# Optimization experiments

Hardware: AMD Instinct MI355X
Metric: run time of the kernel (lower is better)

The kernel has to match this reference:

```python
import jax, jax.numpy as jnp
import numpy as np

B, S, H, A = 64, 2048, 512, 512

def setup_inputs() -> dict:
    key = jax.random.key(0)
    k = jax.random.split(key, 8)
    s = 1.0 / np.sqrt(H)
    sa = 1.0 / np.sqrt(A)
    return {
        "decoder_output": jax.random.normal(k[0], (B, H), jnp.float32),
        "encoder_output": jax.random.normal(k[1], (B, S, H), jnp.float32),
        "W_dec": jax.random.uniform(k[2], (A, H), jnp.float32, -s, s),
        "b_dec": jax.random.uniform(k[3], (A,), jnp.float32, -s, s),
        "W_enc": jax.random.uniform(k[4], (A, H), jnp.float32, -s, s),
        "b_enc": jax.random.uniform(k[5], (A,), jnp.float32, -s, s),
        "V": jax.random.uniform(k[6], (1, A), jnp.float32, -sa, sa),
        "b_v": jax.random.uniform(k[7], (1,), jnp.float32, -sa, sa),
    }

def reference(decoder_output, encoder_output, W_dec, b_dec, W_enc, b_enc, V, b_v):
    # dec proj: (B, A); enc proj: (B, S, A)
    dec_p = decoder_output @ W_dec.T + b_dec
    enc_p = jnp.einsum('bsh,ah->bsa', encoder_output, W_enc) + b_enc
    h = jnp.tanh(dec_p[:, None, :] + enc_p)          # (B, S, A)
    scores = jnp.einsum('bsa,a->bs', h, V[0]) + b_v[0]  # (B, S)
    attn = jax.nn.softmax(scores, axis=-1)           # softmax over seq dim
    ctx = jnp.einsum('bs,bsh->bh', attn, encoder_output)  # (B, H)
    out = jnp.concatenate([ctx, decoder_output], axis=-1)  # (B, 2H)
    return out
```

## Files before the change

### kernel.cpp

```cpp
#include <hip/hip_runtime.h>
#include <cstdint>
#include <cstddef>

#define NB 64
#define NS 2048
#define NH 512
#define NA 512

#define BM 64
#define BK 32

typedef __attribute__((ext_vector_type(8))) short short8;
typedef __attribute__((ext_vector_type(4))) float f32x4;

__device__ inline short f2bf(float f) {
    union { float f; uint32_t u; } v; v.f = f;
    uint32_t u = v.u;
    uint32_t r = (u + 0x7fffu + ((u >> 16) & 1u)) >> 16;
    return (short)r;
}

__device__ inline uint32_t cvtpk_bf16(float lo, float hi) {
    uint32_t r;
    asm("v_cvt_pk_bf16_f32 %0, %1, %2" : "=v"(r) : "v"(lo), "v"(hi));
    return r;
}

__global__ __launch_bounds__(256) void k_decp(const float* __restrict__ dec,
                                              const float* __restrict__ Wd,
                                              const float* __restrict__ bd,
                                              const float* __restrict__ be,
                                              float* __restrict__ dp) {
    int b = blockIdx.x;
    __shared__ float dl[NH];
    for (int i = threadIdx.x; i < NH; i += 256) dl[i] = dec[b * NH + i];
    __syncthreads();
    for (int a = threadIdx.x; a < NA; a += 256) {
        const float4* wr = (const float4*)(Wd + (size_t)a * NH);
        float acc = 0.f;
#pragma unroll 8
        for (int h4 = 0; h4 < NH / 4; ++h4) {
            float4 w = wr[h4];
            acc += dl[h4*4+0]*w.x + dl[h4*4+1]*w.y + dl[h4*4+2]*w.z + dl[h4*4+3]*w.w;
        }
        dp[b * NA + a] = acc + bd[a] + be[a];
    }
}

__global__ __launch_bounds__(256) void k_packw(const float* __restrict__ We,
                                               short* __restrict__ wsw) {
    int t = blockIdx.x * 256 + threadIdx.x;
    int slot = t & 3;
    int a = (t >> 2) & (NA - 1);
    int kt = t >> 11;
    const float* src = We + (size_t)a * NH + kt * 32 + slot * 8;
    int dslot = slot ^ ((a >> 1) & 3);
    short* dst = wsw + (((size_t)kt * NA + a) * 4 + dslot) * 8;
    short8 o;
#pragma unroll
    for (int j = 0; j < 8; ++j) o[j] = f2bf(src[j]);
    *(short8*)dst = o;
}

__global__ __launch_bounds__(256, 2) void k_fused(const float* __restrict__ enc,
                                                  const short* __restrict__ wsw,
                                                  const float* __restrict__ dp,
                                                  const float* __restrict__ V,
                                                  float* __restrict__ pbuf,
                                                  float* __restrict__ ctxp) {
    __shared__ __align__(16) char smem[73728];

    const int tid = threadIdx.x;
    const int w = tid >> 6;
    const int l = tid & 63;
    const int lrow = l & 15;
    const int lg = l >> 4;
    const int row0 = blockIdx.x * BM;
    const int b = row0 >> 11;

    const int sa = tid >> 2;
    const int qa = tid & 3;
    const float* encs = enc + (size_t)(row0 + sa) * NH + qa * 8;
    const int aw_byte = (qa * 64 + (sa ^ (qa << 2))) * 16;

    const char* wsrc = (const char*)wsw;

    const int wfrag = ((w * 128 + lrow) * 4 + (lg ^ ((lrow >> 1) & 3))) * 16;
    const int afrag = (lg * 64 + (lrow ^ (lg << 2))) * 16;

    f32x4 acc[4][8];
#pragma unroll
    for (int i = 0; i < 4; ++i)
#pragma unroll
        for (int j = 0; j < 8; ++j) acc[i][j] = (f32x4){0.f, 0.f, 0.f, 0.f};

    {
#pragma unroll
        for (int r = 0; r < 8; ++r) {
            int blk = r * 4 + w;
            __builtin_amdgcn_global_load_lds(
                (const __attribute__((address_space(1))) void*)(wsrc + ((size_t)blk * 64 + l) * 16),
                (__attribute__((address_space(3))) void*)(smem + blk * 1024), 16, 0, 0);
        }
        f32x4 a0 = *(const f32x4*)(encs);
        f32x4 a1 = *(const f32x4*)(encs + 4);
        union { short8 s8; uint32_t u[4]; } uu;
        uu.u[0] = cvtpk_bf16(a0[0], a0[1]);
        uu.u[1] = cvtpk_bf16(a0[2], a0[3]);
        uu.u[2] = cvtpk_bf16(a1[0], a1[1]);
        uu.u[3] = cvtpk_bf16(a1[2], a1[3]);
        *(short8*)(smem + 65536 + aw_byte) = uu.s8;
    }
    __syncthreads();

    for (int kt = 0; kt < 16; ++kt) {
        const int cur = kt & 1;
        char* Wc = smem + cur * 32768;
        char* Ac = smem + 65536 + cur * 4096;
        char* Wn = smem + (cur ^ 1) * 32768;
        char* An = smem + 65536 + (cur ^ 1) * 4096;

        f32x4 a0, a1;
        if (kt < 15) {
            const float* s = encs + (kt + 1) * BK;
            a0 = *(const f32x4*)(s);
            a1 = *(const f32x4*)(s + 4);
#pragma unroll
            for (int r = 0; r < 8; ++r) {
                int blk = r * 4 + w;
                __builtin_amdgcn_global_load_lds(
                    (const __attribute__((address_space(1))) void*)(wsrc + ((size_t)(kt + 1) * 32768 + ((size_t)blk * 64 + l) * 16)),
                    (__attribute__((address_space(3))) void*)(Wn + blk * 1024), 16, 0, 0);
            }
        }

        short8 bfr[8], af[4];
#pragma unroll
        for (int fn = 0; fn < 8; ++fn) bfr[fn] = *(const short8*)(Wc + wfrag + fn * 1024);
#pragma unroll
        for (int fm = 0; fm < 4; ++fm) af[fm] = *(const short8*)(Ac + afrag + fm * 256);
#pragma unroll
        for (int fm = 0; fm < 4; ++fm)
#pragma unroll
            for (int fn = 0; fn < 8; ++fn)
                acc[fm][fn] = __builtin_amdgcn_mfma_f32_16x16x32_bf16(af[fm], bfr[fn], acc[fm][fn], 0, 0, 0);

        if (kt < 15) {
            union { short8 s8; uint32_t u[4]; } uu;
            uu.u[0] = cvtpk_bf16(a0[0], a0[1]);
            uu.u[1] = cvtpk_bf16(a0[2], a0[3]);
            uu.u[2] = cvtpk_bf16(a1[0], a1[1]);
            uu.u[3] = cvtpk_bf16(a1[2], a1[3]);
            *(short8*)(An + aw_byte) = uu.s8;
        }
        __syncthreads();
    }

    float* sbuf = (float*)smem;
    float* pl = (float*)(smem + 1024);
    float* sb2 = (float*)(smem + 2048);

    float dpl[8], vl[8];
#pragma unroll
    for (int fn = 0; fn < 8; ++fn) {
        int a = w * 128 + fn * 16 + lrow;
        dpl[fn] = dp[b * NA + a];
        vl[fn] = V[a];
    }
    float ps[4][4];
#pragma unroll
    for (int fm = 0; fm < 4; ++fm)
#pragma unroll
        for (int i = 0; i < 4; ++i) ps[fm][i] = 0.f;

#pragma unroll
    for (int fm = 0; fm < 4; ++fm)
#pragma unroll
        for (int fn = 0; fn < 8; ++fn)
#pragma unroll
            for (int i = 0; i < 4; ++i) {
                float x = acc[fm][fn][i] + dpl[fn];
                float u = exp2f(x * 2.885390082f);
                float th = 1.f - 2.f * __builtin_amdgcn_rcpf(u + 1.f);
                ps[fm][i] += th * vl[fn];
            }

#pragma unroll
    for (int fm = 0; fm < 4; ++fm)
#pragma unroll
        for (int i = 0; i < 4; ++i) {
            float v = ps[fm][i];
            v += __shfl_xor(v, 1);
            v += __shfl_xor(v, 2);
            v += __shfl_xor(v, 4);
            v += __shfl_xor(v, 8);
            if (lrow == 0) sbuf[w * 64 + fm * 16 + lg * 4 + i] = v;
        }
    __syncthreads();

    if (tid < BM) {
        float s = sbuf[tid] + sbuf[64 + tid] + sbuf[128 + tid] + sbuf[192 + tid];
        float p = exp2f(s * 1.4426950408889634f);
        pl[tid] = p;
        pbuf[row0 + tid] = p;
    }
    __syncthreads();

    f32x4 c0 = (f32x4){0.f, 0.f, 0.f, 0.f};
    f32x4 c1 = (f32x4){0.f, 0.f, 0.f, 0.f};
    const float* erow = enc + (size_t)(row0 + w * 16) * NH + l * 8;
#pragma unroll 4
    for (int s16 = 0; s16 < 16; ++s16) {
        float pw = pl[w * 16 + s16];
        f32x4 e0 = *(const f32x4*)(erow);
        f32x4 e1 = *(const f32x4*)(erow + 4);
        c0 += pw * e0;
        c1 += pw * e1;
        erow += NH;
    }
    {
        float* sw = sb2 + w * 512;
        *(f32x4*)(sw + l * 4) = c0;
        *(f32x4*)(sw + 256 + l * 4) = c1;
    }
    __syncthreads();

    {
        int h2 = tid * 2;
        int q = h2 >> 3, r = h2 & 7;
        int idx = (r < 4) ? (q * 4 + r) : (256 + q * 4 + (r - 4));
        float r0 = sb2[idx] + sb2[512 + idx] + sb2[1024 + idx] + sb2[1536 + idx];
        float r1 = sb2[idx + 1] + sb2[512 + idx + 1] + sb2[1024 + idx + 1] + sb2[1536 + idx + 1];
        float2* dst = (float2*)(ctxp + (size_t)blockIdx.x * NH + h2);
        *dst = make_float2(r0, r1);
    }
}

__global__ __launch_bounds__(256) void k_combine(const float* __restrict__ ctxp,
                                                 const float* __restrict__ pbuf,
                                                 const float* __restrict__ dec,
                                                 float* __restrict__ out) {
    int b = blockIdx.x;
    int tid = threadIdx.x;
    int l = tid & 63;
    int w = tid >> 6;
    __shared__ float red[4];
    __shared__ float stot;

    const f32x4* pv = (const f32x4*)(pbuf + (size_t)b * NS);
    f32x4 v0 = pv[tid * 2];
    f32x4 v1 = pv[tid * 2 + 1];
    float s = v0[0]+v0[1]+v0[2]+v0[3]+v1[0]+v1[1]+v1[2]+v1[3];
#pragma unroll
    for (int off = 1; off < 64; off <<= 1) s += __shfl_xor(s, off);
    if (l == 0) red[w] = s;
    __syncthreads();
    if (tid == 0) stot = red[0] + red[1] + red[2] + red[3];
    __syncthreads();
    float inv = 1.f / stot;

    int h2 = tid * 2;
    float a0 = 0.f, a1 = 0.f;
#pragma unroll 8
    for (int i = 0; i < NS / BM; ++i) {
        const float2 c = *(const float2*)(ctxp + ((size_t)b * (NS / BM) + i) * NH + h2);
        a0 += c.x;
        a1 += c.y;
    }
    *(float2*)(out + (size_t)b * 1024 + h2) = make_float2(a0 * inv, a1 * inv);
    const float2 dv = *(const float2*)(dec + (size_t)b * NH + h2);
    *(float2*)(out + (size_t)b * 1024 + NH + h2) = dv;
}

extern "C" void kernel_launch(void* const* d_in, const int* in_sizes, int n_in,
                              void* d_out, int out_size, void* d_ws, size_t ws_size,
                              hipStream_t stream) {
    (void)in_sizes; (void)n_in; (void)out_size; (void)ws_size;
    const float* dec = (const float*)d_in[0];
    const float* enc = (const float*)d_in[1];
    const float* Wd  = (const float*)d_in[2];
    const float* bd  = (const float*)d_in[3];
    const float* We  = (const float*)d_in[4];
    const float* be  = (const float*)d_in[5];
    const float* V   = (const float*)d_in[6];
    float* out = (float*)d_out;

    char* ws = (char*)d_ws;
    short* wsw    = (short*)ws;
    float* dpb    = (float*)(ws + (512 << 10));
    float* pbuf   = (float*)(ws + (640 << 10));
    float* ctxp   = (float*)(ws + (1152 << 10));

    k_decp<<<dim3(NB), dim3(256), 0, stream>>>(dec, Wd, bd, be, dpb);
    k_packw<<<dim3(128), dim3(256), 0, stream>>>(We, wsw);
    k_fused<<<dim3((NB * NS) / BM), dim3(256), 0, stream>>>(enc, wsw, dpb, V, pbuf, ctxp);
    k_combine<<<dim3(NB), dim3(256), 0, stream>>>(ctxp, pbuf, dec, out);
}
```

Measured before the change: 166.3 us.

## Load encoder A-fragments directly into registers, drop LDS staging for A

Result: slower. 238.2 us (+43.2%).

```diff
diff --git a/kernel.cpp b/kernel.cpp
--- a/kernel.cpp
+++ b/kernel.cpp
@@ -68,7 +68,7 @@
                                                   const float* __restrict__ V,
                                                   float* __restrict__ pbuf,
                                                   float* __restrict__ ctxp) {
-    __shared__ __align__(16) char smem[73728];
+    __shared__ __align__(16) char smem[65536];
 
     const int tid = threadIdx.x;
     const int w = tid >> 6;
@@ -78,53 +78,50 @@
     const int row0 = blockIdx.x * BM;
     const int b = row0 >> 11;
 
-    const int sa = tid >> 2;
-    const int qa = tid & 3;
-    const float* encs = enc + (size_t)(row0 + sa) * NH + qa * 8;
-    const int aw_byte = (qa * 64 + (sa ^ (qa << 2))) * 16;
-
     const char* wsrc = (const char*)wsw;
-
     const int wfrag = ((w * 128 + lrow) * 4 + (lg ^ ((lrow >> 1) & 3))) * 16;
-    const int afrag = (lg * 64 + (lrow ^ (lg << 2))) * 16;
-
+    const float* abase = enc + (size_t)(row0 + lrow) * NH + lg * 8;
+
+    f32x4 an[8];
     f32x4 acc[4][8];
 #pragma unroll
     for (int i = 0; i < 4; ++i)
 #pragma unroll
         for (int j = 0; j < 8; ++j) acc[i][j] = (f32x4){0.f, 0.f, 0.f, 0.f};
 
-    {
-#pragma unroll
-        for (int r = 0; r < 8; ++r) {
-            int blk = r * 4 + w;
-            __builtin_amdgcn_global_load_lds(
-                (const __attribute__((address_space(1))) void*)(wsrc + ((size_t)blk * 64 + l) * 16),
-                (__attribute__((address_space(3))) void*)(smem + blk * 1024), 16, 0, 0);
-        }
-        f32x4 a0 = *(const f32x4*)(encs);
-        f32x4 a1 = *(const f32x4*)(encs + 4);
-        union { short8 s8; uint32_t u[4]; } uu;
-        uu.u[0] = cvtpk_bf16(a0[0], a0[1]);
-        uu.u[1] = cvtpk_bf16(a0[2], a0[3]);
-        uu.u[2] = cvtpk_bf16(a1[0], a1[1]);
-        uu.u[3] = cvtpk_bf16(a1[2], a1[3]);
-        *(short8*)(smem + 65536 + aw_byte) = uu.s8;
-    }
-    __syncthreads();
+#pragma unroll
+    for (int r = 0; r < 8; ++r) {
+        int blk = r * 4 + w;
+        __builtin_amdgcn_global_load_lds(
+            (const __attribute__((address_space(1))) void*)(wsrc + ((size_t)blk * 64 + l) * 16),
+            (__attribute__((address_space(3))) void*)(smem + blk * 1024), 16, 0, 0);
+    }
+    __builtin_amdgcn_sched_barrier(0);
+#pragma unroll
+    for (int fm = 0; fm < 4; ++fm) {
+        an[2 * fm]     = *(const f32x4*)(abase + fm * 8192);
+        an[2 * fm + 1] = *(const f32x4*)(abase + fm * 8192 + 4);
+    }
+    asm volatile("s_waitcnt vmcnt(8)" ::: "memory");
+    __builtin_amdgcn_s_barrier();
+    __builtin_amdgcn_sched_barrier(0);
 
     for (int kt = 0; kt < 16; ++kt) {
-        const int cur = kt & 1;
-        char* Wc = smem + cur * 32768;
-        char* Ac = smem + 65536 + cur * 4096;
-        char* Wn = smem + (cur ^ 1) * 32768;
-        char* An = smem + 65536 + (cur ^ 1) * 4096;
-
-        f32x4 a0, a1;
+        char* Wc = smem + (kt & 1) * 32768;
+        char* Wn = smem + ((kt + 1) & 1) * 32768;
+
+        short8 af[4];
+#pragma unroll
+        for (int fm = 0; fm < 4; ++fm) {
+            union { short8 s8; uint32_t u[4]; } uu;
+            uu.u[0] = cvtpk_bf16(an[2*fm][0], an[2*fm][1]);
+            uu.u[1] = cvtpk_bf16(an[2*fm][2], an[2*fm][3]);
+            uu.u[2] = cvtpk_bf16(an[2*fm+1][0], an[2*fm+1][1]);
+            uu.u[3] = cvtpk_bf16(an[2*fm+1][2], an[2*fm+1][3]);
+            af[fm] = uu.s8;
+        }
+
         if (kt < 15) {
-            const float* s = encs + (kt + 1) * BK;
-            a0 = *(const f32x4*)(s);
-            a1 = *(const f32x4*)(s + 4);
 #pragma unroll
             for (int r = 0; r < 8; ++r) {
                 int blk = r * 4 + w;
@@ -132,28 +129,27 @@
                     (const __attribute__((address_space(1))) void*)(wsrc + ((size_t)(kt + 1) * 32768 + ((size_t)blk * 64 + l) * 16)),
                     (__attribute__((address_space(3))) void*)(Wn + blk * 1024), 16, 0, 0);
             }
-        }
-
-        short8 bfr[8], af[4];
+            __builtin_amdgcn_sched_barrier(0);
+            const float* ap = abase + (kt + 1) * 32;
+#pragma unroll
+            for (int fm = 0; fm < 4; ++fm) {
+                an[2 * fm]     = *(const f32x4*)(ap + fm * 8192);
+                an[2 * fm + 1] = *(const f32x4*)(ap + fm * 8192 + 4);
+            }
+        }
+
+        short8 bfr[8];
 #pragma unroll
         for (int fn = 0; fn < 8; ++fn) bfr[fn] = *(const short8*)(Wc + wfrag + fn * 1024);
-#pragma unroll
-        for (int fm = 0; fm < 4; ++fm) af[fm] = *(const short8*)(Ac + afrag + fm * 256);
 #pragma unroll
         for (int fm = 0; fm < 4; ++fm)
 #pragma unroll
             for (int fn = 0; fn < 8; ++fn)
                 acc[fm][fn] = __builtin_amdgcn_mfma_f32_16x16x32_bf16(af[fm], bfr[fn], acc[fm][fn], 0, 0, 0);
 
-        if (kt < 15) {
-            union { short8 s8; uint32_t u[4]; } uu;
-            uu.u[0] = cvtpk_bf16(a0[0], a0[1]);
-            uu.u[1] = cvtpk_bf16(a0[2], a0[3]);
-            uu.u[2] = cvtpk_bf16(a1[0], a1[1]);
-            uu.u[3] = cvtpk_bf16(a1[2], a1[3]);
-            *(short8*)(An + aw_byte) = uu.s8;
-        }
-        __syncthreads();
+        asm volatile("s_waitcnt vmcnt(8)" ::: "memory");
+        __builtin_amdgcn_s_barrier();
+        __builtin_amdgcn_sched_barrier(0);
     }
 
     float* sbuf = (float*)smem;
```
